# Performance work log

Hardware: AMD Instinct MI355X
Metric: run time of the kernel (lower is better)

The kernel has to match this reference:

```python
import jax, jax.numpy as jnp
import numpy as np

N_NODES = 100_000
N_EDGES = 1_000_000
D_IN = 64
D_OUT = 64
N_TYPES = 16  # get_options().in_dim; must exceed gate types 9/11 referenced in source


def setup_inputs() -> dict:
    key = jax.random.key(0)
    k = jax.random.split(key, 6)
    feat = jax.random.normal(k[0], (N_NODES, D_IN), dtype=jnp.float32)
    src = jax.random.randint(k[1], (N_EDGES,), 0, N_NODES, dtype=jnp.int32)
    dst = jax.random.randint(k[2], (N_EDGES,), 0, N_NODES, dtype=jnp.int32)
    ntype2 = jax.random.randint(k[3], (N_NODES,), 0, N_TYPES, dtype=jnp.int32)
    # per-type Linear params; xavier-uniform-ish (gain=sqrt(2) for relu)
    limit = np.sqrt(2.0) * np.sqrt(6.0 / (D_IN + D_OUT))
    gate_W = jax.random.uniform(k[4], (N_TYPES, D_IN, D_OUT), jnp.float32, -limit, limit)
    gate_b = jax.random.uniform(k[5], (N_TYPES, D_OUT), jnp.float32, -0.1, 0.1)
    return {"feat": feat, "gate_W": gate_W, "gate_b": gate_b,
            "src": src, "dst": dst, "ntype2": ntype2, "act_flag": 1}


def reference(feat, gate_W, gate_b, src, dst, ntype2, act_flag):
    n = feat.shape[0]
    # update_all(copy_src('h','m'), mean('m','neigh')): gather + segment-mean
    msg = feat[src]                                                  # [E, D_in]
    summed = jax.ops.segment_sum(msg, dst, num_segments=n)           # [N, D_in]
    deg = jax.ops.segment_sum(jnp.ones_like(dst, dtype=feat.dtype), dst, num_segments=n)
    neigh = summed / jnp.maximum(deg, 1.0)[:, None]                  # zero-degree -> 0 (DGL default)
    # apply_nodes_func: route each node through Linear_t with t = ntype2[node]
    # compute all T small GEMMs, then select per node (T is small and fixed)
    out_all = jnp.einsum('nd,tdo->nto', neigh, gate_W) + gate_b[None, :, :]   # [N, T, D_out]
    rst = jnp.take_along_axis(out_all, ntype2.astype(jnp.int32)[:, None, None], axis=1)[:, 0, :]
    # activation is None in this configuration, so act_flag is a no-op
    return rst
```

## Files before the change

### kernel.cpp

```cpp
#include <hip/hip_runtime.h>

#define N_NODES 100000
#define N_EDGES 1000000
#define D 64
#define N_TYPES 16

#define NPB 128
#define NBUCK ((N_NODES + NPB - 1) / NPB)
#define NBLK 256
#define CHUNK 3908
#define NQUAD (CHUNK / 4)
#define ECAP 1520
#define HCAP 1024

#define AWIN 2048
#define ABLKS ((N_NODES + AWIN - 1) / AWIN)
#define LCAP 256

#define WS_TBL    0
#define WS_BTOT   (WS_TBL + NBUCK * NBLK)
#define WS_BSTART (WS_BTOT + NBUCK)
#define WS_EBUF   (WS_BSTART + NBUCK + 1)
#define WS_TOTAL  (WS_EBUF + N_EDGES + 64)

__device__ __forceinline__ float lane_bcast(float v, int l) {
    return __uint_as_float(__builtin_amdgcn_readlane(__float_as_uint(v), l));
}

__global__ void __launch_bounds__(256)
hist_edges(const int* __restrict__ dst, int* __restrict__ tbl) {
    __shared__ int hb[NBUCK];
    int b = blockIdx.x, tid = threadIdx.x;
    for (int i = tid; i < NBUCK; i += 256) hb[i] = 0;
    __syncthreads();
    int beg = b * CHUNK, end = min(beg + CHUNK, N_EDGES);
    for (int e = beg + tid; e < end; e += 256)
        atomicAdd(&hb[dst[e] >> 7], 1);
    __syncthreads();
    for (int i = tid; i < NBUCK; i += 256) tbl[i * NBLK + b] = hb[i];
}

__global__ void __launch_bounds__(512)
scan_cols(int* __restrict__ tbl, int* __restrict__ btot) {
    int wave = blockIdx.x * 8 + (threadIdx.x >> 6);
    int lane = threadIdx.x & 63;
    if (wave >= NBUCK) return;
    int4 v = ((int4*)(tbl + wave * NBLK))[lane];
    int s01 = v.x + v.y;
    int s = s01 + v.z + v.w;
    int incl = s;
    for (int o = 1; o < 64; o <<= 1) {
        int u = __shfl_up(incl, o, 64);
        if (lane >= o) incl += u;
    }
    int excl = incl - s;
    int4 w;
    w.x = excl; w.y = excl + v.x; w.z = excl + s01; w.w = excl + s01 + v.z;
    ((int4*)(tbl + wave * NBLK))[lane] = w;
    if (lane == 63) btot[wave] = incl;
}

__global__ void __launch_bounds__(1024)
scan_buckets(const int* __restrict__ btot, int* __restrict__ bstart) {
    __shared__ int sh[1024];
    int t = threadIdx.x;
    int v = (t < NBUCK) ? btot[t] : 0;
    sh[t] = v;
    __syncthreads();
    for (int o = 1; o < 1024; o <<= 1) {
        int u = (t >= o) ? sh[t - o] : 0;
        __syncthreads();
        sh[t] += u;
        __syncthreads();
    }
    if (t <= NBUCK) bstart[t] = sh[t] - v;
}

__global__ void __launch_bounds__(1024)
place_bucketed(const int* __restrict__ src, const int* __restrict__ dst,
               const int* __restrict__ tbl, const int* __restrict__ bstart,
               unsigned* __restrict__ ebuf) {
    __shared__ int hb[NBUCK];
    __shared__ int lo[NBUCK];
    __shared__ int gb[NBUCK];
    __shared__ int cur[NBUCK];
    __shared__ unsigned short stage_bk[CHUNK];
    __shared__ unsigned stage_ls[CHUNK];
    __shared__ int wpart[16];

    int b = blockIdx.x, tid = threadIdx.x;
    int lane = tid & 63, wv = tid >> 6;
    for (int i = tid; i < NBUCK; i += 1024) hb[i] = 0;
    __syncthreads();

    int beg = b * CHUNK;
    int e0 = beg + 4 * tid;
    int4 d4 = make_int4(-1, -1, -1, -1);
    if (tid < NQUAD && e0 < N_EDGES) {
        if (e0 + 3 < N_EDGES) {
            d4 = ((const int4*)(dst + beg))[tid];
        } else {
            d4.x = dst[e0];
            if (e0 + 1 < N_EDGES) d4.y = dst[e0 + 1];
            if (e0 + 2 < N_EDGES) d4.z = dst[e0 + 2];
        }
    }
    if (d4.x >= 0) atomicAdd(&hb[d4.x >> 7], 1);
    if (d4.y >= 0) atomicAdd(&hb[d4.y >> 7], 1);
    if (d4.z >= 0) atomicAdd(&hb[d4.z >> 7], 1);
    if (d4.w >= 0) atomicAdd(&hb[d4.w >> 7], 1);
    __syncthreads();

    int v = (tid < NBUCK) ? hb[tid] : 0;
    int incl = v;
    for (int o = 1; o < 64; o <<= 1) {
        int u = __shfl_up(incl, o, 64);
        if (lane >= o) incl += u;
    }
    if (lane == 63) wpart[wv] = incl;
    __syncthreads();
    if (tid == 0) {
        int r = 0;
        for (int w = 0; w < 16; ++w) { int t = wpart[w]; wpart[w] = r; r += t; }
    }
    __syncthreads();
    incl += wpart[wv];
    int excl = incl - v;
    if (tid < NBUCK) { lo[tid] = excl; cur[tid] = excl; }
    __syncthreads();

    int4 s4 = make_int4(0, 0, 0, 0);
    if (tid < NQUAD && e0 < N_EDGES) {
        if (e0 + 3 < N_EDGES) {
            s4 = ((const int4*)(src + beg))[tid];
        } else {
            s4.x = src[e0];
            if (e0 + 1 < N_EDGES) s4.y = src[e0 + 1];
            if (e0 + 2 < N_EDGES) s4.z = src[e0 + 2];
        }
    }
    if (d4.x >= 0) { int bk = d4.x >> 7; int p = atomicAdd(&cur[bk], 1);
                     stage_bk[p] = (unsigned short)bk;
                     stage_ls[p] = ((unsigned)(d4.x & 127) << 20) | (unsigned)s4.x; }
    if (d4.y >= 0) { int bk = d4.y >> 7; int p = atomicAdd(&cur[bk], 1);
                     stage_bk[p] = (unsigned short)bk;
                     stage_ls[p] = ((unsigned)(d4.y & 127) << 20) | (unsigned)s4.y; }
    if (d4.z >= 0) { int bk = d4.z >> 7; int p = atomicAdd(&cur[bk], 1);
                     stage_bk[p] = (unsigned short)bk;
                     stage_ls[p] = ((unsigned)(d4.z & 127) << 20) | (unsigned)s4.z; }
    if (d4.w >= 0) { int bk = d4.w >> 7; int p = atomicAdd(&cur[bk], 1);
                     stage_bk[p] = (unsigned short)bk;
                     stage_ls[p] = ((unsigned)(d4.w & 127) << 20) | (unsigned)s4.w; }

    if (tid < NBUCK)
        gb[tid] = bstart[tid] + tbl[tid * NBLK + b] - lo[tid];
    __syncthreads();

    int end = min(beg + CHUNK, N_EDGES);
    int cnt = end - beg;
    for (int idx = tid; idx < cnt; idx += 1024) {
        int bk = (int)stage_bk[idx];
        ebuf[gb[bk] + idx] = stage_ls[idx];
    }
}

__global__ void __launch_bounds__(256)
bucket_gather(const float* __restrict__ feat, const int* __restrict__ bstart,
              const unsigned* __restrict__ ebuf, float* __restrict__ out) {
    __shared__ int hist[64], offL[64], curL[64];
    __shared__ unsigned eL[ECAP];
    __shared__ int sortedL[HCAP];

    int blk = blockIdx.x, tid = threadIdx.x;
    int bucket = blk >> 1, half = blk & 1;
    int base = bstart[bucket];
    int ecnt = bstart[bucket + 1] - base;
    if (ecnt > ECAP) ecnt = ECAP;
    if (tid < 64) hist[tid] = 0;
    __syncthreads();

    for (int i = tid; i < ecnt; i += 256) {
        unsigned p = ebuf[base + i];
        eL[i] = p;
        if (((p >> 26) & 1u) == (unsigned)half)
            atomicAdd(&hist[(p >> 20) & 63], 1);
    }
    __syncthreads();
    if (tid < 64) {
        int v = hist[tid];
        int incl = v;
        for (int o = 1; o < 64; o <<= 1) {
            int u = __shfl_up(incl, o, 64);
            if (tid >= o) incl += u;
        }
        offL[tid] = incl - v;
        curL[tid] = incl - v;
    }
    __syncthreads();
    for (int i = tid; i < ecnt; i += 256) {
        unsigned p = eL[i];
        if (((p >> 26) & 1u) == (unsigned)half) {
            int pos = atomicAdd(&curL[(p >> 20) & 63], 1);
            if (pos < HCAP) sortedL[pos] = (int)(p & 0xFFFFFu);
        }
    }
    __syncthreads();

    int hw = tid >> 5, h = tid & 31;
    const float2* __restrict__ F = (const float2*)feat;
    int node0 = bucket * NPB + half * 64;
#pragma unroll
    for (int it = 0; it < 8; ++it) {
        int nl = hw * 8 + it;
        int cnt = hist[nl], o = offL[nl];
        float sx = 0.0f, sy = 0.0f;
        int j = 0;
        for (; j + 4 <= cnt; j += 4) {
            int s0 = sortedL[o + j + 0];
            int s1 = sortedL[o + j + 1];
            int s2 = sortedL[o + j + 2];
            int s3 = sortedL[o + j + 3];
            float2 v0 = F[s0 * 32 + h];
            float2 v1 = F[s1 * 32 + h];
            float2 v2 = F[s2 * 32 + h];
            float2 v3 = F[s3 * 32 + h];
            sx += (v0.x + v1.x) + (v2.x + v3.x);
            sy += (v0.y + v1.y) + (v2.y + v3.y);
        }
        for (; j < cnt; ++j) {
            int s = sortedL[o + j];
            float2 v = F[s * 32 + h];
            sx += v.x; sy += v.y;
        }
        int node = node0 + nl;
        if (node < N_NODES) {
            float scale = (cnt > 1) ? (1.0f / (float)cnt) : 1.0f;
            float2 r; r.x = sx * scale; r.y = sy * scale;
            ((float2*)out)[node * 32 + h] = r;
        }
    }
}

__global__ void __launch_bounds__(512, 2)
type_apply(const float* __restrict__ gate_W, const float* __restrict__ gate_b,
           const int* __restrict__ ntype2, float* __restrict__ out) {
    __shared__ int list[LCAP];
    __shared__ int lcnt;

    int tid = threadIdx.x, lane = tid & 63, wv = tid >> 6;
    int t = blockIdx.x & 15;
    int n0 = (blockIdx.x >> 4) * AWIN;
    if (tid == 0) lcnt = 0;
    __syncthreads();
    for (int i = tid; i < AWIN; i += 512) {
        int n = n0 + i;
        if (n < N_NODES && ntype2[n] == t) {
            int p = atomicAdd(&lcnt, 1);
            if (p < LCAP) list[p] = n;
        }
    }
    __syncthreads();
    int cnt = min(lcnt, LCAP);
    if (cnt == 0) return;

    const float* __restrict__ W = gate_W + t * D * D;
    float wreg[D];
#pragma unroll
    for (int d = 0; d < D; ++d) wreg[d] = W[d * D + lane];
    float bias = gate_b[t * D + lane];

    for (int i = wv; i < cnt; i += 8) {
        int n = list[i];
        float r = out[n * D + lane];
        float a0 = bias, a1 = 0.0f, a2 = 0.0f, a3 = 0.0f;
#pragma unroll
        for (int d = 0; d < D; d += 4) {
            a0 = fmaf(lane_bcast(r, d + 0), wreg[d + 0], a0);
            a1 = fmaf(lane_bcast(r, d + 1), wreg[d + 1], a1);
            a2 = fmaf(lane_bcast(r, d + 2), wreg[d + 2], a2);
            a3 = fmaf(lane_bcast(r, d + 3), wreg[d + 3], a3);
        }
        out[n * D + lane] = (a0 + a1) + (a2 + a3);
    }
}

__global__ void scatter_feat(const float* __restrict__ feat, const int* __restrict__ src,
                             const int* __restrict__ dst, float* __restrict__ accum) {
    long long idx = (long long)blockIdx.x * blockDim.x + threadIdx.x;
    if (idx >= (long long)N_EDGES * D) return;
    int e = (int)(idx >> 6), d = (int)(idx & 63);
    atomicAdd(accum + dst[e] * D + d, feat[src[e] * D + d]);
}
__global__ void scatter_deg(const int* __restrict__ dst, float* __restrict__ deg) {
    int e = blockIdx.x * blockDim.x + threadIdx.x;
    if (e >= N_EDGES) return;
    atomicAdd(deg + dst[e], 1.0f);
}
__global__ void apply_linear(const float* __restrict__ gate_W, const float* __restrict__ gate_b,
                             const int* __restrict__ ntype2, const float* __restrict__ deg,
                             float* __restrict__ out) {
    int node = blockIdx.x * (blockDim.x >> 6) + (threadIdx.x >> 6);
    int lane = threadIdx.x & 63;
    if (node >= N_NODES) return;
    int t = ntype2[node];
    float dv = deg[node]; dv = dv > 1.0f ? dv : 1.0f;
    float nv = out[node * D + lane] / dv;
    const float* W = gate_W + t * D * D;
    float acc = gate_b[t * D + lane];
#pragma unroll 16
    for (int d = 0; d < D; ++d)
        acc = fmaf(__shfl(nv, d, 64), W[d * D + lane], acc);
    out[node * D + lane] = acc;
}

extern "C" void kernel_launch(void* const* d_in, const int* in_sizes, int n_in,
                              void* d_out, int out_size, void* d_ws, size_t ws_size,
                              hipStream_t stream) {
    const float* feat   = (const float*)d_in[0];
    const float* gate_W = (const float*)d_in[1];
    const float* gate_b = (const float*)d_in[2];
    const int*   src    = (const int*)d_in[3];
    const int*   dst    = (const int*)d_in[4];
    const int*   ntype2 = (const int*)d_in[5];
    float* out = (float*)d_out;

    if (ws_size >= (size_t)WS_TOTAL * 4) {
        int* ws = (int*)d_ws;
        int* tbl       = ws + WS_TBL;
        int* btot      = ws + WS_BTOT;
        int* bstart    = ws + WS_BSTART;
        unsigned* ebuf = (unsigned*)(ws + WS_EBUF);

        hist_edges<<<NBLK, 256, 0, stream>>>(dst, tbl);
        scan_cols<<<(NBUCK + 7) / 8, 512, 0, stream>>>(tbl, btot);
        scan_buckets<<<1, 1024, 0, stream>>>(btot, bstart);
        place_bucketed<<<NBLK, 1024, 0, stream>>>(src, dst, tbl, bstart, ebuf);
        bucket_gather<<<NBUCK * 2, 256, 0, stream>>>(feat, bstart, ebuf, out);
        type_apply<<<ABLKS * 16, 512, 0, stream>>>(gate_W, gate_b, ntype2, out);
    } else {
        float* deg = (float*)d_ws;
        hipMemsetAsync(out, 0, sizeof(float) * N_NODES * D, stream);
        hipMemsetAsync(deg, 0, sizeof(float) * N_NODES, stream);
        long long total = (long long)N_EDGES * D;
        scatter_feat<<<(int)((total + 255) / 256), 256, 0, stream>>>(feat, src, dst, out);
        scatter_deg<<<(N_EDGES + 255) / 256, 256, 0, stream>>>(dst, deg);
        apply_linear<<<(N_NODES + 3) / 4, 256, 0, stream>>>(gate_W, gate_b, ntype2, deg, out);
    }
}
```

Measured before the change: 176.4 us.

## Merge scan kernels via last-block pattern, split gather into quarter-buckets, shrink apply blocks

Fuses the column scan and the bucket scan into one kernel. The last block to finish, detected with an atomic counter in workspace, computes the bucket prefix, which removes one launch. The gather kernel now splits each 128-node bucket into four 32-node windows instead of two halves, and maps blocks in a strided order. It drops the shared copy of the edge list and rereads ebuf from global instead, trading extra global reads for smaller shared memory and more blocks. The type-apply kernel uses 256-thread blocks with a smaller node window.

```diff
diff --git a/kernel.cpp b/kernel.cpp
--- a/kernel.cpp
+++ b/kernel.cpp
@@ -10,17 +10,21 @@
 #define NBLK 256
 #define CHUNK 3908
 #define NQUAD (CHUNK / 4)
-#define ECAP 1520
-#define HCAP 1024
-
-#define AWIN 2048
+
+#define GWIN 32
+#define GBLK (NBUCK * 4)
+#define GCPX (GBLK / 8)
+#define SCAP 512
+
+#define AWIN 1024
 #define ABLKS ((N_NODES + AWIN - 1) / AWIN)
-#define LCAP 256
+#define LCAP 160
 
 #define WS_TBL    0
 #define WS_BTOT   (WS_TBL + NBUCK * NBLK)
 #define WS_BSTART (WS_BTOT + NBUCK)
 #define WS_EBUF   (WS_BSTART + NBUCK + 1)
+#define WS_CNT    (WS_EBUF + N_EDGES)
 #define WS_TOTAL  (WS_EBUF + N_EDGES + 64)
 
 __device__ __forceinline__ float lane_bcast(float v, int l) {
@@ -28,9 +32,10 @@
 }
 
 __global__ void __launch_bounds__(256)
-hist_edges(const int* __restrict__ dst, int* __restrict__ tbl) {
+hist_edges(const int* __restrict__ dst, int* __restrict__ tbl, int* __restrict__ cnt) {
     __shared__ int hb[NBUCK];
     int b = blockIdx.x, tid = threadIdx.x;
+    if (b == 0 && tid == 0) cnt[0] = 0;
     for (int i = tid; i < NBUCK; i += 256) hb[i] = 0;
     __syncthreads();
     int beg = b * CHUNK, end = min(beg + CHUNK, N_EDGES);
@@ -41,39 +46,54 @@
 }
 
 __global__ void __launch_bounds__(512)
-scan_cols(int* __restrict__ tbl, int* __restrict__ btot) {
-    int wave = blockIdx.x * 8 + (threadIdx.x >> 6);
-    int lane = threadIdx.x & 63;
-    if (wave >= NBUCK) return;
-    int4 v = ((int4*)(tbl + wave * NBLK))[lane];
-    int s01 = v.x + v.y;
-    int s = s01 + v.z + v.w;
+scan_all(int* __restrict__ tbl, int* __restrict__ btot,
+         int* __restrict__ bstart, int* __restrict__ cnt) {
+    __shared__ int islast;
+    __shared__ int wpart[8];
+    int tid = threadIdx.x, lane = tid & 63, wv = tid >> 6;
+    int wave = blockIdx.x * 8 + wv;
+    if (wave < NBUCK) {
+        int4 v = ((int4*)(tbl + wave * NBLK))[lane];
+        int s01 = v.x + v.y;
+        int s = s01 + v.z + v.w;
+        int incl = s;
+        for (int o = 1; o < 64; o <<= 1) {
+            int u = __shfl_up(incl, o, 64);
+            if (lane >= o) incl += u;
+        }
+        int excl = incl - s;
+        int4 w;
+        w.x = excl; w.y = excl + v.x; w.z = excl + s01; w.w = excl + s01 + v.z;
+        ((int4*)(tbl + wave * NBLK))[lane] = w;
+        if (lane == 63) btot[wave] = incl;
+    }
+    __threadfence();
+    __syncthreads();
+    if (tid == 0) islast = (atomicAdd(cnt, 1) == (int)gridDim.x - 1);
+    __syncthreads();
+    if (!islast) return;
+    __threadfence();
+    int i0 = 2 * tid, i1 = i0 + 1;
+    int a0 = (i0 < NBUCK) ? btot[i0] : 0;
+    int a1 = (i1 < NBUCK) ? btot[i1] : 0;
+    int s = a0 + a1;
     int incl = s;
     for (int o = 1; o < 64; o <<= 1) {
         int u = __shfl_up(incl, o, 64);
         if (lane >= o) incl += u;
     }
+    if (lane == 63) wpart[wv] = incl;
+    __syncthreads();
+    if (tid == 0) {
+        int r = 0;
+        for (int w = 0; w < 8; ++w) { int t = wpart[w]; wpart[w] = r; r += t; }
+    }
+    __syncthreads();
+    incl += wpart[wv];
     int excl = incl - s;
-    int4 w;
-    w.x = excl; w.y = excl + v.x; w.z = excl + s01; w.w = excl + s01 + v.z;
-    ((int4*)(tbl + wave * NBLK))[lane] = w;
-    if (lane == 63) btot[wave] = incl;
-}
-
-__global__ void __launch_bounds__(1024)
-scan_buckets(const int* __restrict__ btot, int* __restrict__ bstart) {
-    __shared__ int sh[1024];
-    int t = threadIdx.x;
-    int v = (t < NBUCK) ? btot[t] : 0;
-    sh[t] = v;
-    __syncthreads();
-    for (int o = 1; o < 1024; o <<= 1) {
-        int u = (t >= o) ? sh[t - o] : 0;
-        __syncthreads();
-        sh[t] += u;
-        __syncthreads();
-    }
-    if (t <= NBUCK) bstart[t] = sh[t] - v;
+    if (i0 < NBUCK) bstart[i0] = excl;
+    if (i1 < NBUCK) bstart[i1] = excl + a0;
+    if (tid == 0) bstart[NBUCK] = N_EDGES;
 }
 
 __global__ void __launch_bounds__(1024)
@@ -167,29 +187,28 @@
 __global__ void __launch_bounds__(256)
 bucket_gather(const float* __restrict__ feat, const int* __restrict__ bstart,
               const unsigned* __restrict__ ebuf, float* __restrict__ out) {
-    __shared__ int hist[64], offL[64], curL[64];
-    __shared__ unsigned eL[ECAP];
-    __shared__ int sortedL[HCAP];
-
-    int blk = blockIdx.x, tid = threadIdx.x;
-    int bucket = blk >> 1, half = blk & 1;
+    __shared__ int hist[GWIN], offL[GWIN], curL[GWIN];
+    __shared__ int sortedL[SCAP];
+
+    int L = blockIdx.x, tid = threadIdx.x;
+    int m = (L & 7) * GCPX + (L >> 3);
+    int bucket = m >> 2;
+    unsigned q = (unsigned)(m & 3);
     int base = bstart[bucket];
     int ecnt = bstart[bucket + 1] - base;
-    if (ecnt > ECAP) ecnt = ECAP;
-    if (tid < 64) hist[tid] = 0;
+    if (tid < GWIN) hist[tid] = 0;
     __syncthreads();
 
     for (int i = tid; i < ecnt; i += 256) {
         unsigned p = ebuf[base + i];
-        eL[i] = p;
-        if (((p >> 26) & 1u) == (unsigned)half)
-            atomicAdd(&hist[(p >> 20) & 63], 1);
-    }
-    __syncthreads();
-    if (tid < 64) {
+        if (((p >> 25) & 3u) == q)
+            atomicAdd(&hist[(p >> 20) & 31], 1);
+    }
+    __syncthreads();
+    if (tid < GWIN) {
         int v = hist[tid];
         int incl = v;
-        for (int o = 1; o < 64; o <<= 1) {
+        for (int o = 1; o < GWIN; o <<= 1) {
             int u = __shfl_up(incl, o, 64);
             if (tid >= o) incl += u;
         }
@@ -198,20 +217,20 @@
     }
     __syncthreads();
     for (int i = tid; i < ecnt; i += 256) {
-        unsigned p = eL[i];
-        if (((p >> 26) & 1u) == (unsigned)half) {
-            int pos = atomicAdd(&curL[(p >> 20) & 63], 1);
-            if (pos < HCAP) sortedL[pos] = (int)(p & 0xFFFFFu);
+        unsigned p = ebuf[base + i];
+        if (((p >> 25) & 3u) == q) {
+            int pos = atomicAdd(&curL[(p >> 20) & 31], 1);
+            if (pos < SCAP) sortedL[pos] = (int)(p & 0xFFFFFu);
         }
     }
     __syncthreads();
 
     int hw = tid >> 5, h = tid & 31;
     const float2* __restrict__ F = (const float2*)feat;
-    int node0 = bucket * NPB + half * 64;
+    int node0 = bucket * NPB + (int)q * GWIN;
 #pragma unroll
-    for (int it = 0; it < 8; ++it) {
-        int nl = hw * 8 + it;
+    for (int it = 0; it < 4; ++it) {
+        int nl = hw * 4 + it;
         int cnt = hist[nl], o = offL[nl];
         float sx = 0.0f, sy = 0.0f;
         int j = 0;
@@ -241,7 +260,7 @@
     }
 }
 
-__global__ void __launch_bounds__(512, 2)
+__global__ void __launch_bounds__(256)
 type_apply(const float* __restrict__ gate_W, const float* __restrict__ gate_b,
            const int* __restrict__ ntype2, float* __restrict__ out) {
     __shared__ int list[LCAP];
@@ -252,7 +271,7 @@
     int n0 = (blockIdx.x >> 4) * AWIN;
     if (tid == 0) lcnt = 0;
     __syncthreads();
-    for (int i = tid; i < AWIN; i += 512) {
+    for (int i = tid; i < AWIN; i += 256) {
         int n = n0 + i;
         if (n < N_NODES && ntype2[n] == t) {
             int p = atomicAdd(&lcnt, 1);
@@ -269,7 +288,7 @@
     for (int d = 0; d < D; ++d) wreg[d] = W[d * D + lane];
     float bias = gate_b[t * D + lane];
 
-    for (int i = wv; i < cnt; i += 8) {
+    for (int i = wv; i < cnt; i += 4) {
         int n = list[i];
         float r = out[n * D + lane];
         float a0 = bias, a1 = 0.0f, a2 = 0.0f, a3 = 0.0f;
@@ -330,13 +349,13 @@
         int* btot      = ws + WS_BTOT;
         int* bstart    = ws + WS_BSTART;
         unsigned* ebuf = (unsigned*)(ws + WS_EBUF);
-
-        hist_edges<<<NBLK, 256, 0, stream>>>(dst, tbl);
-        scan_cols<<<(NBUCK + 7) / 8, 512, 0, stream>>>(tbl, btot);
-        scan_buckets<<<1, 1024, 0, stream>>>(btot, bstart);
+        int* cnt       = ws + WS_CNT;
+
+        hist_edges<<<NBLK, 256, 0, stream>>>(dst, tbl, cnt);
+        scan_all<<<(NBUCK + 7) / 8, 512, 0, stream>>>(tbl, btot, bstart, cnt);
         place_bucketed<<<NBLK, 1024, 0, stream>>>(src, dst, tbl, bstart, ebuf);
-        bucket_gather<<<NBUCK * 2, 256, 0, stream>>>(feat, bstart, ebuf, out);
-        type_apply<<<ABLKS * 16, 512, 0, stream>>>(gate_W, gate_b, ntype2, out);
+        bucket_gather<<<GBLK, 256, 0, stream>>>(feat, bstart, ebuf, out);
+        type_apply<<<ABLKS * 16, 256, 0, stream>>>(gate_W, gate_b, ntype2, out);
     } else {
         float* deg = (float*)d_ws;
         hipMemsetAsync(out, 0, sizeof(float) * N_NODES * D, stream);
```

Result: slower. 194.9 us (+10.5%).

## Fuse per-type linear apply into bucket gather kernel

Applied to the files above, without the earlier changes.

Removes the separate type_apply kernel and performs the per-node typed Linear inside bucket_gather. Mean-aggregated rows are kept in shared memory, nodes are sorted by type within each 64-node block, and each wave computes outputs for 16 nodes, reloading weights when the type changes. This removes a global round trip of the intermediate and one launch, but adds shared memory per block (lower occupancy) and frequent weight reloads from cache.

```diff
diff --git a/kernel.cpp b/kernel.cpp
--- a/kernel.cpp
+++ b/kernel.cpp
@@ -13,19 +13,11 @@
 #define ECAP 1520
 #define HCAP 1024
 
-#define AWIN 2048
-#define ABLKS ((N_NODES + AWIN - 1) / AWIN)
-#define LCAP 256
-
 #define WS_TBL    0
 #define WS_BTOT   (WS_TBL + NBUCK * NBLK)
 #define WS_BSTART (WS_BTOT + NBUCK)
 #define WS_EBUF   (WS_BSTART + NBUCK + 1)
 #define WS_TOTAL  (WS_EBUF + N_EDGES + 64)
-
-__device__ __forceinline__ float lane_bcast(float v, int l) {
-    return __uint_as_float(__builtin_amdgcn_readlane(__float_as_uint(v), l));
-}
 
 __global__ void __launch_bounds__(256)
 hist_edges(const int* __restrict__ dst, int* __restrict__ tbl) {
@@ -166,10 +158,16 @@
 
 __global__ void __launch_bounds__(256)
 bucket_gather(const float* __restrict__ feat, const int* __restrict__ bstart,
-              const unsigned* __restrict__ ebuf, float* __restrict__ out) {
+              const unsigned* __restrict__ ebuf,
+              const float* __restrict__ gate_W, const float* __restrict__ gate_b,
+              const int* __restrict__ ntype2, float* __restrict__ out) {
     __shared__ int hist[64], offL[64], curL[64];
     __shared__ unsigned eL[ECAP];
     __shared__ int sortedL[HCAP];
+    __shared__ float rowfull[64 * D];
+    __shared__ unsigned char ord[64];
+    __shared__ unsigned char typ[64];
+    __shared__ int tc[N_TYPES], tcur[N_TYPES];
 
     int blk = blockIdx.x, tid = threadIdx.x;
     int bucket = blk >> 1, half = blk & 1;
@@ -209,6 +207,9 @@
     int hw = tid >> 5, h = tid & 31;
     const float2* __restrict__ F = (const float2*)feat;
     int node0 = bucket * NPB + half * 64;
+    int nvalid = N_NODES - node0;
+    if (nvalid > 64) nvalid = 64;
+    if (nvalid < 0) nvalid = 0;
 #pragma unroll
     for (int it = 0; it < 8; ++it) {
         int nl = hw * 8 + it;
@@ -232,55 +233,54 @@
             float2 v = F[s * 32 + h];
             sx += v.x; sy += v.y;
         }
-        int node = node0 + nl;
-        if (node < N_NODES) {
-            float scale = (cnt > 1) ? (1.0f / (float)cnt) : 1.0f;
-            float2 r; r.x = sx * scale; r.y = sy * scale;
-            ((float2*)out)[node * 32 + h] = r;
-        }
-    }
-}
-
-__global__ void __launch_bounds__(512, 2)
-type_apply(const float* __restrict__ gate_W, const float* __restrict__ gate_b,
-           const int* __restrict__ ntype2, float* __restrict__ out) {
-    __shared__ int list[LCAP];
-    __shared__ int lcnt;
-
-    int tid = threadIdx.x, lane = tid & 63, wv = tid >> 6;
-    int t = blockIdx.x & 15;
-    int n0 = (blockIdx.x >> 4) * AWIN;
-    if (tid == 0) lcnt = 0;
-    __syncthreads();
-    for (int i = tid; i < AWIN; i += 512) {
-        int n = n0 + i;
-        if (n < N_NODES && ntype2[n] == t) {
-            int p = atomicAdd(&lcnt, 1);
-            if (p < LCAP) list[p] = n;
-        }
-    }
-    __syncthreads();
-    int cnt = min(lcnt, LCAP);
-    if (cnt == 0) return;
-
-    const float* __restrict__ W = gate_W + t * D * D;
+        float scale = (cnt > 1) ? (1.0f / (float)cnt) : 1.0f;
+        float2 r; r.x = sx * scale; r.y = sy * scale;
+        ((float2*)rowfull)[nl * 32 + h] = r;
+    }
+
+    if (tid < N_TYPES) tc[tid] = 0;
+    __syncthreads();
+    int myt = -1;
+    if (tid < nvalid) { myt = ntype2[node0 + tid]; atomicAdd(&tc[myt], 1); }
+    __syncthreads();
+    if (tid == 0) {
+        int r = 0;
+        for (int t = 0; t < N_TYPES; ++t) { int cc = tc[t]; tcur[t] = r; r += cc; }
+    }
+    __syncthreads();
+    if (tid < nvalid) {
+        int p = atomicAdd(&tcur[myt], 1);
+        ord[p] = (unsigned char)tid;
+        typ[p] = (unsigned char)myt;
+    }
+    __syncthreads();
+
+    int lane = tid & 63, wv = tid >> 6;
+    int i0 = wv * 16, i1 = i0 + 16; if (i1 > nvalid) i1 = nvalid;
+    int tprev = -1;
     float wreg[D];
+    float bias = 0.0f;
+    for (int i = i0; i < i1; ++i) {
+        int n = (int)ord[i];
+        int t = (int)typ[i];
+        if (t != tprev) {
+            tprev = t;
+            const float* __restrict__ W = gate_W + t * D * D;
 #pragma unroll
-    for (int d = 0; d < D; ++d) wreg[d] = W[d * D + lane];
-    float bias = gate_b[t * D + lane];
-
-    for (int i = wv; i < cnt; i += 8) {
-        int n = list[i];
-        float r = out[n * D + lane];
+            for (int d = 0; d < D; ++d) wreg[d] = W[d * D + lane];
+            bias = gate_b[t * D + lane];
+        }
+        const float* __restrict__ ar = &rowfull[n * D];
         float a0 = bias, a1 = 0.0f, a2 = 0.0f, a3 = 0.0f;
 #pragma unroll
         for (int d = 0; d < D; d += 4) {
-            a0 = fmaf(lane_bcast(r, d + 0), wreg[d + 0], a0);
-            a1 = fmaf(lane_bcast(r, d + 1), wreg[d + 1], a1);
-            a2 = fmaf(lane_bcast(r, d + 2), wreg[d + 2], a2);
-            a3 = fmaf(lane_bcast(r, d + 3), wreg[d + 3], a3);
-        }
-        out[n * D + lane] = (a0 + a1) + (a2 + a3);
+            float4 av = *(const float4*)(ar + d);
+            a0 = fmaf(av.x, wreg[d + 0], a0);
+            a1 = fmaf(av.y, wreg[d + 1], a1);
+            a2 = fmaf(av.z, wreg[d + 2], a2);
+            a3 = fmaf(av.w, wreg[d + 3], a3);
+        }
+        out[(node0 + n) * D + lane] = (a0 + a1) + (a2 + a3);
     }
 }
 
@@ -335,8 +335,8 @@
         scan_cols<<<(NBUCK + 7) / 8, 512, 0, stream>>>(tbl, btot);
         scan_buckets<<<1, 1024, 0, stream>>>(btot, bstart);
         place_bucketed<<<NBLK, 1024, 0, stream>>>(src, dst, tbl, bstart, ebuf);
-        bucket_gather<<<NBUCK * 2, 256, 0, stream>>>(feat, bstart, ebuf, out);
-        type_apply<<<ABLKS * 16, 512, 0, stream>>>(gate_W, gate_b, ntype2, out);
+        bucket_gather<<<NBUCK * 2, 256, 0, stream>>>(feat, bstart, ebuf,
+                                                     gate_W, gate_b, ntype2, out);
     } else {
         float* deg = (float*)d_ws;
         hipMemsetAsync(out, 0, sizeof(float) * N_NODES * D, stream);
```

After: 175.4 us, median of 2. About the same (-0.6%).
